# Kernel tuning notes

Measured on AMD Instinct MI355X. Metric: run time of the kernel, lower is better.

## Reference

```python
import jax, jax.numpy as jnp
import numpy as np

B, T, H, I, OUT = 128, 1440, 512, 2, 1
TAU, ALPHA = 6.0, 0.1


def setup_inputs() -> dict:
    key = jax.random.key(0)
    ks = jax.random.split(key, 8)
    xs = jax.random.normal(ks[0], (B, T), dtype=jnp.float32)
    # sparse 0/1 observation mask (channel 2); channel 1 unused by forward
    mask = (jax.random.uniform(ks[1], (B, T)) < 0.05).astype(jnp.float32)
    inp = jnp.stack([xs, jnp.zeros((B, T), jnp.float32), mask], axis=1)[..., None]  # [B,3,T,1]
    s = 1.0 / np.sqrt(H)
    u = lambda k, shp: jax.random.uniform(k, shp, minval=-s, maxval=s, dtype=jnp.float32)
    return {
        "input": inp,
        "w_ih": u(ks[2], (3 * H, I)),
        "w_hh": u(ks[3], (3 * H, H)),
        "b_ih": u(ks[4], (3 * H,)),
        "b_hh": u(ks[5], (3 * H,)),
        "w_fc": u(ks[6], (OUT, H)),
        "b_fc": u(ks[7], (OUT,)),
    }


def belief_fill(x, mask, half_tau):
    # Vectorized equivalent of the per-batch / per-observed-index Python loop:
    # each position takes the value of the next observed index if within half_tau
    # else the previous observed index if within half_tau, else stays unchanged.
    Ts = x.shape[1]
    t = jnp.arange(Ts)[None, :]
    obs = mask == 1
    p = jax.lax.cummax(jnp.where(obs, t, -1), axis=1)                       # prev observed idx or -1
    n = jax.lax.cummin(jnp.where(obs, t, Ts)[:, ::-1], axis=1)[:, ::-1]      # next observed idx or Ts
    xp = jnp.take_along_axis(x, jnp.clip(p, 0, Ts - 1), axis=1)
    xn = jnp.take_along_axis(x, jnp.clip(n, 0, Ts - 1), axis=1)
    use_n = (n < Ts) & (t >= n - half_tau)
    use_p = (p >= 0) & (t <= p + half_tau)
    return jnp.where(use_n, xn, jnp.where(use_p, xp, x))


def _forward(inp, w_ih, w_hh, b_ih, b_hh, w_fc, b_fc):
    xs = inp[:, 0, :, 0]      # [B,T]
    masks = inp[:, 2, :, 0]   # [B,T]
    xs = jnp.where(jnp.isnan(xs), -1.0, xs)
    # tau update: old_weight is ones(3H, I)
    grads = jnp.mean(w_ih - 1.0)
    tau_new = TAU + grads * ALPHA
    trigger = (tau_new >= 1.0) & (tau_new != TAU)
    half_tau = jnp.round(tau_new / 2.0)
    xs = jnp.where(trigger, belief_fill(xs, masks, half_tau), xs)
    gru_in = jnp.stack((xs, masks), axis=2)  # [B,T,2]
    # precompute input projections once (the only input-dependent GEMM)
    gi = jnp.einsum('bti,gi->btg', gru_in, w_ih) + b_ih  # [B,T,3H]

    def step(h, gi_t):
        gh = h @ w_hh.T + b_hh
        r = jax.nn.sigmoid(gi_t[:, :H] + gh[:, :H])
        z = jax.nn.sigmoid(gi_t[:, H:2 * H] + gh[:, H:2 * H])
        ng = jnp.tanh(gi_t[:, 2 * H:] + r * gh[:, 2 * H:])
        h = (1.0 - z) * ng + z * h
        return h, None

    h0 = jnp.zeros((inp.shape[0], H), gi.dtype)
    h_last, _ = jax.lax.scan(step, h0, jnp.swapaxes(gi, 0, 1))
    return h_last @ w_fc.T + b_fc  # [B, OUT]


def reference(input, w_ih, w_hh, b_ih, b_hh, w_fc, b_fc):
    return _forward(input, w_ih, w_hh, b_ih, b_hh, w_fc, b_fc)
```

## Files before the change

### kernel.cpp

```cpp
#include <hip/hip_runtime.h>
#include <math.h>

#define BN   128
#define TN   1440
#define HN   512
#define GBn  8
#define BSn  16
#define GCn  32
#define HCn  16
#define WST  536

using f16 = _Float16;
typedef f16   f16x8 __attribute__((ext_vector_type(8)));
typedef float f32x4 __attribute__((ext_vector_type(4)));
typedef unsigned int       uint32;
typedef unsigned long long u64;

#define OFF_SCAL 1024
#define OFF_HBUF 2048
#define OFF_XSF  (2048 + 2 * BN * HN * 4)

__global__ void k_prep(const float* __restrict__ w_ih, float* __restrict__ scal) {
    __shared__ float ssum[4];
    float s = 0.0f;
    for (int i = threadIdx.x; i < 3 * HN * 2; i += 256) s += w_ih[i];
    for (int o = 32; o >= 1; o >>= 1) s += __shfl_down(s, o, 64);
    if ((threadIdx.x & 63) == 0) ssum[threadIdx.x >> 6] = s;
    __syncthreads();
    if (threadIdx.x == 0) {
        float tot = ssum[0] + ssum[1] + ssum[2] + ssum[3];
        float grads = tot / 3072.0f - 1.0f;
        float tau_new = 6.0f + grads * 0.1f;
        bool trig = (tau_new >= 1.0f) && (tau_new != 6.0f);
        scal[0] = rintf(tau_new * 0.5f);
        scal[1] = trig ? 1.0f : 0.0f;
    }
}

__global__ void k_fill(const float* __restrict__ inp, const float* __restrict__ scal,
                       float* __restrict__ xsf) {
    const int b = blockIdx.x;
    const int lane = threadIdx.x;
    const float ht = scal[0];
    const bool trig = scal[1] != 0.0f;
    const float* xrow = inp + (size_t)b * 3 * TN;
    const float* mrow = xrow + 2 * TN;
    const int CH = 23;
    const int start = lane * CH;

    if (!trig) {
        for (int i = 0; i < CH; ++i) {
            int t = start + i;
            if (t < TN) { float x = xrow[t]; if (x != x) x = -1.0f; xsf[(size_t)b * TN + t] = x; }
        }
        return;
    }
    int pm = -1;
#pragma unroll
    for (int i = 0; i < CH; ++i) { int t = start + i; if (t < TN && mrow[t] == 1.0f) pm = t; }
    int incl = pm;
    for (int o = 1; o < 64; o <<= 1) { int v = __shfl_up(incl, o, 64); if (lane >= o) incl = max(incl, v); }
    int pexcl = __shfl_up(incl, 1, 64); if (lane == 0) pexcl = -1;
    int nm = TN;
#pragma unroll
    for (int i = CH - 1; i >= 0; --i) { int t = start + i; if (t < TN && mrow[t] == 1.0f) nm = t; }
    int incl2 = nm;
    for (int o = 1; o < 64; o <<= 1) { int v = __shfl_down(incl2, o, 64); if (lane + o < 64) incl2 = min(incl2, v); }
    int nexcl = __shfl_down(incl2, 1, 64); if (lane == 63) nexcl = TN;
    int narr[23];
    int runn = nexcl;
#pragma unroll
    for (int i = CH - 1; i >= 0; --i) {
        int t = start + i;
        if (t < TN) { if (mrow[t] == 1.0f) runn = t; narr[i] = runn; } else narr[i] = TN;
    }
    int runp = pexcl;
#pragma unroll
    for (int i = 0; i < CH; ++i) {
        int t = start + i;
        if (t >= TN) break;
        float x = xrow[t]; if (x != x) x = -1.0f;
        if (mrow[t] == 1.0f) runp = t;
        int pv = runp, nv = narr[i];
        int pc = min(max(pv, 0), TN - 1), nc = min(max(nv, 0), TN - 1);
        float xp = xrow[pc]; if (xp != xp) xp = -1.0f;
        float xn = xrow[nc]; if (xn != xn) xn = -1.0f;
        bool use_n = (nv < TN) && ((float)t >= (float)nv - ht);
        bool use_p = (pv >= 0) && ((float)t <= (float)pv + ht);
        float o = use_n ? xn : (use_p ? xp : x);
        xsf[(size_t)b * TN + t] = o;
    }
}

__global__ __launch_bounds__(256, 1) void k_gru(
    const float* __restrict__ inp, const float* __restrict__ w_ih,
    const float* __restrict__ w_hh, const float* __restrict__ b_ih,
    const float* __restrict__ b_hh, const float* __restrict__ w_fc,
    const float* __restrict__ b_fc, const float* __restrict__ xsf,
    uint32* __restrict__ hbufP, int* __restrict__ flags, float* __restrict__ out) {
    __shared__ __align__(16) f16 sHhi[BSn * WST];
    __shared__ __align__(16) f16 sHlo[BSn * WST];
    __shared__ float sGh[3][BSn][HCn + 1];
    __shared__ float sWi0[48], sWi1[48], sBias[48];

    const int tid = threadIdx.x;
    const int gb = blockIdx.x & 7;
    const int gc = blockIdx.x >> 3;
    const int lane = tid & 63;
    const int wv   = tid >> 6;
    const int bs   = tid >> 4;
    const int j    = tid & 15;
    const int bglob = gb * BSn + bs;
    const int pcol  = gc * HCn + j;
    const int frow = lane & 15;
    const int kgrp = lane >> 4;

    if (tid < 48) {
        int gate = tid >> 4, jj = tid & 15;
        int grow = gate * HN + gc * HCn + jj;
        sWi0[tid]  = w_ih[grow * 2 + 0];
        sWi1[tid]  = w_ih[grow * 2 + 1];
        sBias[tid] = b_ih[grow] + b_hh[grow];
    }

    f16x8 bfh[16], bfl[16];
    if (wv < 3) {
        const float* wrow = w_hh + (size_t)(wv * HN + gc * HCn + frow) * HN;
#pragma unroll
        for (int c = 0; c < 16; ++c) {
            const int k0 = (c * 4 + kgrp) * 8;
#pragma unroll
            for (int u = 0; u < 8; ++u) {
                float w = wrow[k0 + u];
                f16 hi = (f16)w;
                bfh[c][u] = hi;
                bfl[c][u] = (f16)((w - (float)hi) * 2048.0f);
            }
        }
    }
    __syncthreads();

    int* myflags = flags + gb * GCn;
    const f16x8* pAhi = (const f16x8*)(sHhi + frow * WST);
    const f16x8* pAlo = (const f16x8*)(sHlo + frow * WST);
    float h = 0.0f;

    for (int t = 0; t < TN; ++t) {
        float xsv = xsf[(size_t)bglob * TN + t];
        float mkv = inp[((size_t)bglob * 3 + 2) * TN + t];
        if (lane < GCn) {
            while (__hip_atomic_load(&myflags[lane], __ATOMIC_RELAXED, __HIP_MEMORY_SCOPE_AGENT) < t) {}
        }
        {
            const uint32* src = hbufP + ((size_t)(t & 1) * BN + gb * BSn) * HN;
            u64 hv[16];
#pragma unroll
            for (int i = 0; i < 16; ++i)
                hv[i] = __hip_atomic_load((const u64*)(src + (size_t)i * HN) + tid,
                                          __ATOMIC_RELAXED, __HIP_MEMORY_SCOPE_AGENT);
#pragma unroll
            for (int i = 0; i < 16; ++i) {
                uint32 d0 = (uint32)hv[i], d1 = (uint32)(hv[i] >> 32);
                ((uint32*)(sHhi + i * WST))[tid] = __builtin_amdgcn_perm(d1, d0, 0x05040100u);
                ((uint32*)(sHlo + i * WST))[tid] = __builtin_amdgcn_perm(d1, d0, 0x07060302u);
            }
        }
        __syncthreads();
        if (wv < 3) {
            f32x4 acch = {0.f, 0.f, 0.f, 0.f}, accl = {0.f, 0.f, 0.f, 0.f};
#pragma unroll
            for (int c = 0; c < 16; ++c) {
                f16x8 ah = pAhi[c * 4 + kgrp];
                f16x8 al = pAlo[c * 4 + kgrp];
                acch = __builtin_amdgcn_mfma_f32_16x16x32_f16(ah, bfh[c], acch, 0, 0, 0);
                accl = __builtin_amdgcn_mfma_f32_16x16x32_f16(ah, bfl[c], accl, 0, 0, 0);
                accl = __builtin_amdgcn_mfma_f32_16x16x32_f16(al, bfh[c], accl, 0, 0, 0);
            }
#pragma unroll
            for (int r = 0; r < 4; ++r)
                sGh[wv][kgrp * 4 + r][frow] = acch[r] + accl[r] * (1.0f / 2048.0f);
        }
        __syncthreads();
        {
            float ghr = sGh[0][bs][j], ghz = sGh[1][bs][j], ghn = sGh[2][bs][j];
            float gir = xsv * sWi0[j]      + mkv * sWi1[j]      + sBias[j];
            float giz = xsv * sWi0[16 + j] + mkv * sWi1[16 + j] + sBias[16 + j];
            float gin = xsv * sWi0[32 + j] + mkv * sWi1[32 + j] + sBias[32 + j];
            float rg = 1.0f / (1.0f + __expf(-(gir + ghr)));
            float zg = 1.0f / (1.0f + __expf(-(giz + ghz)));
            float ng = tanhf(gin + rg * ghn);
            h = (1.0f - zg) * ng + zg * h;
            f16 hi = (f16)h;
            f16 lo = (f16)((h - (float)hi) * 2048.0f);
            uint32 pk = (uint32)__builtin_bit_cast(unsigned short, hi)
                      | ((uint32)__builtin_bit_cast(unsigned short, lo) << 16);
            __hip_atomic_store(&hbufP[((size_t)((t + 1) & 1) * BN + bglob) * HN + pcol], pk,
                               __ATOMIC_RELAXED, __HIP_MEMORY_SCOPE_AGENT);
        }
        __syncthreads();
        if (tid == 0)
            __hip_atomic_store(&myflags[gc], t + 1, __ATOMIC_RELAXED, __HIP_MEMORY_SCOPE_AGENT);
    }
    float part = h * w_fc[pcol];
#pragma unroll
    for (int o = 1; o < 16; o <<= 1) part += __shfl_xor(part, o, 64);
    if (j == 0) {
        if (gc == 0) part += b_fc[0];
        atomicAdd(&out[bglob], part);
    }
}

extern "C" void kernel_launch(void* const* d_in, const int* in_sizes, int n_in,
                              void* d_out, int out_size, void* d_ws, size_t ws_size,
                              hipStream_t stream) {
    const float* inp  = (const float*)d_in[0];
    const float* w_ih = (const float*)d_in[1];
    const float* w_hh = (const float*)d_in[2];
    const float* b_ih = (const float*)d_in[3];
    const float* b_hh = (const float*)d_in[4];
    const float* w_fc = (const float*)d_in[5];
    const float* b_fc = (const float*)d_in[6];
    float* out = (float*)d_out;
    char* ws = (char*)d_ws;
    int*    flags = (int*)ws;
    float*  scal  = (float*)(ws + OFF_SCAL);
    uint32* hbufP = (uint32*)(ws + OFF_HBUF);
    float*  xsf   = (float*)(ws + OFF_XSF);

    hipMemsetAsync(ws, 0, OFF_HBUF + BN * HN * 4, stream);
    hipMemsetAsync(d_out, 0, BN * sizeof(float), stream);
    k_prep<<<1, 256, 0, stream>>>(w_ih, scal);
    k_fill<<<BN, 64, 0, stream>>>(inp, scal, xsf);
    k_gru<<<GBn * GCn, 256, 0, stream>>>(inp, w_ih, w_hh, b_ih, b_hh, w_fc, b_fc,
                                         xsf, hbufP, flags, out);
}
```

Baseline: 3.975 ms.

## Replace per-block step flags with tagged hidden-state words for synchronization

Drops the per-block flag array and the spin-wait/flag-store handshake. Each hidden-state word now packs a 24-bit fixed-point value with an 8-bit step tag, and consumers poll the data itself until the tags match, then convert to hi/lo fp16 pairs. This removes one __syncthreads, one flag round-trip per step and the serialized flag polling. The cost is lower precision for h (24-bit fixed point over [-1,1]), extra conversion arithmetic, and reliance on 64-bit atomic loads so that both tags in a word pair are seen together.

```diff
diff --git a/kernel.cpp b/kernel.cpp
--- a/kernel.cpp
+++ b/kernel.cpp
@@ -97,7 +97,7 @@
     const float* __restrict__ w_hh, const float* __restrict__ b_ih,
     const float* __restrict__ b_hh, const float* __restrict__ w_fc,
     const float* __restrict__ b_fc, const float* __restrict__ xsf,
-    uint32* __restrict__ hbufP, int* __restrict__ flags, float* __restrict__ out) {
+    uint32* __restrict__ hbufT, float* __restrict__ out) {
     __shared__ __align__(16) f16 sHhi[BSn * WST];
     __shared__ __align__(16) f16 sHlo[BSn * WST];
     __shared__ float sGh[3][BSn][HCn + 1];
@@ -140,7 +140,6 @@
     }
     __syncthreads();
 
-    int* myflags = flags + gb * GCn;
     const f16x8* pAhi = (const f16x8*)(sHhi + frow * WST);
     const f16x8* pAlo = (const f16x8*)(sHlo + frow * WST);
     float h = 0.0f;
@@ -148,21 +147,39 @@
     for (int t = 0; t < TN; ++t) {
         float xsv = xsf[(size_t)bglob * TN + t];
         float mkv = inp[((size_t)bglob * 3 + 2) * TN + t];
-        if (lane < GCn) {
-            while (__hip_atomic_load(&myflags[lane], __ATOMIC_RELAXED, __HIP_MEMORY_SCOPE_AGENT) < t) {}
-        }
         {
-            const uint32* src = hbufP + ((size_t)(t & 1) * BN + gb * BSn) * HN;
+            const uint32* src = hbufT + ((size_t)(t & 1) * BN + gb * BSn) * HN;
+            const uint32 tagexp = (uint32)(t & 255);
             u64 hv[16];
 #pragma unroll
-            for (int i = 0; i < 16; ++i)
-                hv[i] = __hip_atomic_load((const u64*)(src + (size_t)i * HN) + tid,
+            for (int i = 0; i < 16; ++i) {
+                int row = (i + bs) & 15;
+                hv[i] = __hip_atomic_load((const u64*)(src + (size_t)row * HN) + tid,
                                           __ATOMIC_RELAXED, __HIP_MEMORY_SCOPE_AGENT);
+            }
 #pragma unroll
             for (int i = 0; i < 16; ++i) {
-                uint32 d0 = (uint32)hv[i], d1 = (uint32)(hv[i] >> 32);
-                ((uint32*)(sHhi + i * WST))[tid] = __builtin_amdgcn_perm(d1, d0, 0x05040100u);
-                ((uint32*)(sHlo + i * WST))[tid] = __builtin_amdgcn_perm(d1, d0, 0x07060302u);
+                int row = (i + bs) & 15;
+                while ((((uint32)hv[i] >> 24) != tagexp) ||
+                       (((uint32)(hv[i] >> 32) >> 24) != tagexp)) {
+                    __builtin_amdgcn_s_sleep(1);
+                    hv[i] = __hip_atomic_load((const u64*)(src + (size_t)row * HN) + tid,
+                                              __ATOMIC_RELAXED, __HIP_MEMORY_SCOPE_AGENT);
+                }
+                uint32 a = (uint32)hv[i], b = (uint32)(hv[i] >> 32);
+                int q0 = ((int)(a << 8)) >> 8;
+                int q1 = ((int)(b << 8)) >> 8;
+                float f0 = (float)q0 * 0x1p-23f;
+                float f1 = (float)q1 * 0x1p-23f;
+                f16 h0 = (f16)f0, h1 = (f16)f1;
+                f16 l0 = (f16)((f0 - (float)h0) * 2048.0f);
+                f16 l1 = (f16)((f1 - (float)h1) * 2048.0f);
+                ((uint32*)(sHhi + row * WST))[tid] =
+                    (uint32)__builtin_bit_cast(unsigned short, h0) |
+                    ((uint32)__builtin_bit_cast(unsigned short, h1) << 16);
+                ((uint32*)(sHlo + row * WST))[tid] =
+                    (uint32)__builtin_bit_cast(unsigned short, l0) |
+                    ((uint32)__builtin_bit_cast(unsigned short, l1) << 16);
             }
         }
         __syncthreads();
@@ -190,16 +207,12 @@
             float zg = 1.0f / (1.0f + __expf(-(giz + ghz)));
             float ng = tanhf(gin + rg * ghn);
             h = (1.0f - zg) * ng + zg * h;
-            f16 hi = (f16)h;
-            f16 lo = (f16)((h - (float)hi) * 2048.0f);
-            uint32 pk = (uint32)__builtin_bit_cast(unsigned short, hi)
-                      | ((uint32)__builtin_bit_cast(unsigned short, lo) << 16);
-            __hip_atomic_store(&hbufP[((size_t)((t + 1) & 1) * BN + bglob) * HN + pcol], pk,
+            int q = (int)rintf(h * 8388608.0f);
+            q = min(q, 8388607);
+            uint32 pk = ((uint32)q & 0xFFFFFFu) | (((uint32)(t + 1) & 255u) << 24);
+            __hip_atomic_store(&hbufT[((size_t)((t + 1) & 1) * BN + bglob) * HN + pcol], pk,
                                __ATOMIC_RELAXED, __HIP_MEMORY_SCOPE_AGENT);
         }
-        __syncthreads();
-        if (tid == 0)
-            __hip_atomic_store(&myflags[gc], t + 1, __ATOMIC_RELAXED, __HIP_MEMORY_SCOPE_AGENT);
     }
     float part = h * w_fc[pcol];
 #pragma unroll
@@ -222,9 +235,8 @@
     const float* b_fc = (const float*)d_in[6];
     float* out = (float*)d_out;
     char* ws = (char*)d_ws;
-    int*    flags = (int*)ws;
     float*  scal  = (float*)(ws + OFF_SCAL);
-    uint32* hbufP = (uint32*)(ws + OFF_HBUF);
+    uint32* hbufT = (uint32*)(ws + OFF_HBUF);
     float*  xsf   = (float*)(ws + OFF_XSF);
 
     hipMemsetAsync(ws, 0, OFF_HBUF + BN * HN * 4, stream);
@@ -232,5 +244,5 @@
     k_prep<<<1, 256, 0, stream>>>(w_ih, scal);
     k_fill<<<BN, 64, 0, stream>>>(inp, scal, xsf);
     k_gru<<<GBn * GCn, 256, 0, stream>>>(inp, w_ih, w_hh, b_ih, b_hh, w_fc, b_fc,
-                                         xsf, hbufP, flags, out);
-}
+                                         xsf, hbufT, out);
+}
```

After: 8.464 ms. 113% more time.

## Collapse GRU block to a single wavefront, loading h directly into registers

Applied to the files above, without the earlier changes.

Each GRU block shrinks from four waves to one 64-thread wave. That wave does all three gate GEMMs with MFMA, keeping the high-half weights in registers and the low-half weights in LDS. The hidden state is now read straight from global memory into registers with inline-asm dwordx4 loads that bypass the cache, and written back with one vector store per thread. This removes the LDS staging of h and all per-step __syncthreads, which shortens the serial per-timestep critical path. The cost is that each wave now does three times the MFMA work, register pressure rises sharply, and ordering depends on hand-written waitcnt asm.

```diff
diff --git a/kernel.cpp b/kernel.cpp
--- a/kernel.cpp
+++ b/kernel.cpp
@@ -8,13 +8,13 @@
 #define BSn  16
 #define GCn  32
 #define HCn  16
-#define WST  536
 
 using f16 = _Float16;
 typedef f16   f16x8 __attribute__((ext_vector_type(8)));
 typedef float f32x4 __attribute__((ext_vector_type(4)));
 typedef unsigned int       uint32;
 typedef unsigned long long u64;
+typedef uint32 u32x4 __attribute__((ext_vector_type(4)));
 
 #define OFF_SCAL 1024
 #define OFF_HBUF 2048
@@ -92,28 +92,23 @@
     }
 }
 
-__global__ __launch_bounds__(256, 1) void k_gru(
+__global__ __launch_bounds__(64, 1) void k_gru(
     const float* __restrict__ inp, const float* __restrict__ w_ih,
     const float* __restrict__ w_hh, const float* __restrict__ b_ih,
     const float* __restrict__ b_hh, const float* __restrict__ w_fc,
     const float* __restrict__ b_fc, const float* __restrict__ xsf,
     uint32* __restrict__ hbufP, int* __restrict__ flags, float* __restrict__ out) {
-    __shared__ __align__(16) f16 sHhi[BSn * WST];
-    __shared__ __align__(16) f16 sHlo[BSn * WST];
-    __shared__ float sGh[3][BSn][HCn + 1];
-    __shared__ float sWi0[48], sWi1[48], sBias[48];
-
-    const int tid = threadIdx.x;
-    const int gb = blockIdx.x & 7;
-    const int gc = blockIdx.x >> 3;
-    const int lane = tid & 63;
-    const int wv   = tid >> 6;
-    const int bs   = tid >> 4;
-    const int j    = tid & 15;
-    const int bglob = gb * BSn + bs;
-    const int pcol  = gc * HCn + j;
-    const int frow = lane & 15;
-    const int kgrp = lane >> 4;
+    __shared__ __align__(16) f16x8 sBlo[48 * 65];
+    __shared__ __align__(16) float sGh[3][16][20];
+    __shared__ __align__(16) float sWi0[48], sWi1[48], sBias[48];
+
+    const int tid  = threadIdx.x;
+    const int gb   = blockIdx.x & 7;
+    const int gc   = blockIdx.x >> 3;
+    const int frow = tid & 15;
+    const int kgrp = tid >> 4;
+    const int r    = tid >> 2;
+    const int jq   = (tid & 3) * 4;
 
     if (tid < 48) {
         int gate = tid >> 4, jj = tid & 15;
@@ -123,90 +118,168 @@
         sBias[tid] = b_ih[grow] + b_hh[grow];
     }
 
-    f16x8 bfh[16], bfl[16];
-    if (wv < 3) {
-        const float* wrow = w_hh + (size_t)(wv * HN + gc * HCn + frow) * HN;
+    f16x8 bh[3][16];
+#pragma unroll
+    for (int g = 0; g < 3; ++g) {
+        const float* wrow = w_hh + (size_t)(g * HN + gc * HCn + frow) * HN;
 #pragma unroll
         for (int c = 0; c < 16; ++c) {
             const int k0 = (c * 4 + kgrp) * 8;
+            f16x8 lo;
 #pragma unroll
             for (int u = 0; u < 8; ++u) {
                 float w = wrow[k0 + u];
                 f16 hi = (f16)w;
-                bfh[c][u] = hi;
-                bfl[c][u] = (f16)((w - (float)hi) * 2048.0f);
+                bh[g][c][u] = hi;
+                lo[u] = (f16)((w - (float)hi) * 2048.0f);
             }
-        }
-    }
-    __syncthreads();
+            sBlo[(g * 16 + frow) * 65 + c * 4 + kgrp] = lo;
+        }
+    }
+    asm volatile("s_waitcnt lgkmcnt(0)" ::: "memory");
 
     int* myflags = flags + gb * GCn;
-    const f16x8* pAhi = (const f16x8*)(sHhi + frow * WST);
-    const f16x8* pAlo = (const f16x8*)(sHlo + frow * WST);
-    float h = 0.0f;
+    const uint32* srcA = hbufP + (size_t)(gb * BSn + frow) * HN + kgrp * 8;
+    const uint32* srcB = srcA + (size_t)BN * HN;
+    uint32* dstA = hbufP + (size_t)(gb * BSn + r) * HN + gc * HCn + jq;
+    uint32* dstB = dstA + (size_t)BN * HN;
+    float hv[4] = {0.f, 0.f, 0.f, 0.f};
+    int fcache = 0;
 
     for (int t = 0; t < TN; ++t) {
-        float xsv = xsf[(size_t)bglob * TN + t];
-        float mkv = inp[((size_t)bglob * 3 + 2) * TN + t];
-        if (lane < GCn) {
-            while (__hip_atomic_load(&myflags[lane], __ATOMIC_RELAXED, __HIP_MEMORY_SCOPE_AGENT) < t) {}
-        }
+        float xsv = xsf[(size_t)(gb * BSn + r) * TN + t];
+        float mkv = inp[((size_t)(gb * BSn + r) * 3 + 2) * TN + t];
+        if (tid < GCn) {
+            while (fcache < t)
+                fcache = __hip_atomic_load(&myflags[tid], __ATOMIC_RELAXED,
+                                           __HIP_MEMORY_SCOPE_AGENT);
+        }
+        const uint32* src = (t & 1) ? srcB : srcA;
+        u32x4 L[32];
+        asm volatile(
+            "global_load_dwordx4 %0, %32, off sc0 sc1\n\t"
+            "global_load_dwordx4 %1, %32, off offset:16 sc0 sc1\n\t"
+            "global_load_dwordx4 %2, %32, off offset:128 sc0 sc1\n\t"
+            "global_load_dwordx4 %3, %32, off offset:144 sc0 sc1\n\t"
+            "global_load_dwordx4 %4, %32, off offset:256 sc0 sc1\n\t"
+            "global_load_dwordx4 %5, %32, off offset:272 sc0 sc1\n\t"
+            "global_load_dwordx4 %6, %32, off offset:384 sc0 sc1\n\t"
+            "global_load_dwordx4 %7, %32, off offset:400 sc0 sc1\n\t"
+            "global_load_dwordx4 %8, %32, off offset:512 sc0 sc1\n\t"
+            "global_load_dwordx4 %9, %32, off offset:528 sc0 sc1\n\t"
+            "global_load_dwordx4 %10, %32, off offset:640 sc0 sc1\n\t"
+            "global_load_dwordx4 %11, %32, off offset:656 sc0 sc1\n\t"
+            "global_load_dwordx4 %12, %32, off offset:768 sc0 sc1\n\t"
+            "global_load_dwordx4 %13, %32, off offset:784 sc0 sc1\n\t"
+            "global_load_dwordx4 %14, %32, off offset:896 sc0 sc1\n\t"
+            "global_load_dwordx4 %15, %32, off offset:912 sc0 sc1\n\t"
+            "global_load_dwordx4 %16, %32, off offset:1024 sc0 sc1\n\t"
+            "global_load_dwordx4 %17, %32, off offset:1040 sc0 sc1\n\t"
+            "global_load_dwordx4 %18, %32, off offset:1152 sc0 sc1\n\t"
+            "global_load_dwordx4 %19, %32, off offset:1168 sc0 sc1\n\t"
+            "global_load_dwordx4 %20, %32, off offset:1280 sc0 sc1\n\t"
+            "global_load_dwordx4 %21, %32, off offset:1296 sc0 sc1\n\t"
+            "global_load_dwordx4 %22, %32, off offset:1408 sc0 sc1\n\t"
+            "global_load_dwordx4 %23, %32, off offset:1424 sc0 sc1\n\t"
+            "global_load_dwordx4 %24, %32, off offset:1536 sc0 sc1\n\t"
+            "global_load_dwordx4 %25, %32, off offset:1552 sc0 sc1\n\t"
+            "global_load_dwordx4 %26, %32, off offset:1664 sc0 sc1\n\t"
+            "global_load_dwordx4 %27, %32, off offset:1680 sc0 sc1\n\t"
+            "global_load_dwordx4 %28, %32, off offset:1792 sc0 sc1\n\t"
+            "global_load_dwordx4 %29, %32, off offset:1808 sc0 sc1\n\t"
+            "global_load_dwordx4 %30, %32, off offset:1920 sc0 sc1\n\t"
+            "global_load_dwordx4 %31, %32, off offset:1936 sc0 sc1\n\t"
+            "s_waitcnt vmcnt(0)"
+            : "=&v"(L[0]), "=&v"(L[1]), "=&v"(L[2]), "=&v"(L[3]),
+              "=&v"(L[4]), "=&v"(L[5]), "=&v"(L[6]), "=&v"(L[7]),
+              "=&v"(L[8]), "=&v"(L[9]), "=&v"(L[10]), "=&v"(L[11]),
+              "=&v"(L[12]), "=&v"(L[13]), "=&v"(L[14]), "=&v"(L[15]),
+              "=&v"(L[16]), "=&v"(L[17]), "=&v"(L[18]), "=&v"(L[19]),
+              "=&v"(L[20]), "=&v"(L[21]), "=&v"(L[22]), "=&v"(L[23]),
+              "=&v"(L[24]), "=&v"(L[25]), "=&v"(L[26]), "=&v"(L[27]),
+              "=&v"(L[28]), "=&v"(L[29]), "=&v"(L[30]), "=&v"(L[31])
+            : "v"(src)
+            : "memory");
+        f32x4 acch[3]  = {{0.f,0.f,0.f,0.f},{0.f,0.f,0.f,0.f},{0.f,0.f,0.f,0.f}};
+        f32x4 accl1[3] = {{0.f,0.f,0.f,0.f},{0.f,0.f,0.f,0.f},{0.f,0.f,0.f,0.f}};
+        f32x4 accl2[3] = {{0.f,0.f,0.f,0.f},{0.f,0.f,0.f,0.f},{0.f,0.f,0.f,0.f}};
+#pragma unroll
+        for (int c = 0; c < 16; ++c) {
+            u32x4 a = L[2 * c], b = L[2 * c + 1];
+            u32x4 hq = { __builtin_amdgcn_perm(a.y, a.x, 0x05040100u),
+                         __builtin_amdgcn_perm(a.w, a.z, 0x05040100u),
+                         __builtin_amdgcn_perm(b.y, b.x, 0x05040100u),
+                         __builtin_amdgcn_perm(b.w, b.z, 0x05040100u) };
+            u32x4 lq = { __builtin_amdgcn_perm(a.y, a.x, 0x07060302u),
+                         __builtin_amdgcn_perm(a.w, a.z, 0x07060302u),
+                         __builtin_amdgcn_perm(b.y, b.x, 0x07060302u),
+                         __builtin_amdgcn_perm(b.w, b.z, 0x07060302u) };
+            f16x8 ah = __builtin_bit_cast(f16x8, hq);
+            f16x8 al = __builtin_bit_cast(f16x8, lq);
+#pragma unroll
+            for (int g = 0; g < 3; ++g) {
+                f16x8 bl = sBlo[(g * 16 + frow) * 65 + c * 4 + kgrp];
+                acch[g]  = __builtin_amdgcn_mfma_f32_16x16x32_f16(ah, bh[g][c], acch[g], 0, 0, 0);
+                accl1[g] = __builtin_amdgcn_mfma_f32_16x16x32_f16(ah, bl,       accl1[g], 0, 0, 0);
+                accl2[g] = __builtin_amdgcn_mfma_f32_16x16x32_f16(al, bh[g][c], accl2[g], 0, 0, 0);
+            }
+        }
+#pragma unroll
+        for (int g = 0; g < 3; ++g)
+#pragma unroll
+            for (int q = 0; q < 4; ++q)
+                sGh[g][kgrp * 4 + q][frow] =
+                    acch[g][q] + (accl1[g][q] + accl2[g][q]) * (1.0f / 2048.0f);
+        asm volatile("s_waitcnt lgkmcnt(0)" ::: "memory");
+        float4 gr = *(const float4*)&sGh[0][r][jq];
+        float4 gz = *(const float4*)&sGh[1][r][jq];
+        float4 gn = *(const float4*)&sGh[2][r][jq];
+        float4 w0r = *(const float4*)&sWi0[jq],      w1r = *(const float4*)&sWi1[jq],      bbr = *(const float4*)&sBias[jq];
+        float4 w0z = *(const float4*)&sWi0[16 + jq], w1z = *(const float4*)&sWi1[16 + jq], bbz = *(const float4*)&sBias[16 + jq];
+        float4 w0n = *(const float4*)&sWi0[32 + jq], w1n = *(const float4*)&sWi1[32 + jq], bbn = *(const float4*)&sBias[32 + jq];
+        uint32 pk[4];
         {
-            const uint32* src = hbufP + ((size_t)(t & 1) * BN + gb * BSn) * HN;
-            u64 hv[16];
-#pragma unroll
-            for (int i = 0; i < 16; ++i)
-                hv[i] = __hip_atomic_load((const u64*)(src + (size_t)i * HN) + tid,
-                                          __ATOMIC_RELAXED, __HIP_MEMORY_SCOPE_AGENT);
-#pragma unroll
-            for (int i = 0; i < 16; ++i) {
-                uint32 d0 = (uint32)hv[i], d1 = (uint32)(hv[i] >> 32);
-                ((uint32*)(sHhi + i * WST))[tid] = __builtin_amdgcn_perm(d1, d0, 0x05040100u);
-                ((uint32*)(sHlo + i * WST))[tid] = __builtin_amdgcn_perm(d1, d0, 0x07060302u);
+            const float* grp = (const float*)&gr; const float* gzp = (const float*)&gz;
+            const float* gnp = (const float*)&gn;
+            const float* a0r = (const float*)&w0r; const float* a1r = (const float*)&w1r; const float* abr = (const float*)&bbr;
+            const float* a0z = (const float*)&w0z; const float* a1z = (const float*)&w1z; const float* abz = (const float*)&bbz;
+            const float* a0n = (const float*)&w0n; const float* a1n = (const float*)&w1n; const float* abn = (const float*)&bbn;
+#pragma unroll
+            for (int i = 0; i < 4; ++i) {
+                float gir = fmaf(xsv, a0r[i], fmaf(mkv, a1r[i], abr[i])) + grp[i];
+                float giz = fmaf(xsv, a0z[i], fmaf(mkv, a1z[i], abz[i])) + gzp[i];
+                float gin = fmaf(xsv, a0n[i], fmaf(mkv, a1n[i], abn[i]));
+                float rg = 1.0f / (1.0f + __expf(-gir));
+                float zg = 1.0f / (1.0f + __expf(-giz));
+                float ng = tanhf(gin + rg * gnp[i]);
+                float hn2 = (1.0f - zg) * ng + zg * hv[i];
+                hv[i] = hn2;
+                f16 phi = (f16)hn2;
+                f16 plo = (f16)((hn2 - (float)phi) * 2048.0f);
+                pk[i] = (uint32)__builtin_bit_cast(unsigned short, phi)
+                      | ((uint32)__builtin_bit_cast(unsigned short, plo) << 16);
             }
         }
-        __syncthreads();
-        if (wv < 3) {
-            f32x4 acch = {0.f, 0.f, 0.f, 0.f}, accl = {0.f, 0.f, 0.f, 0.f};
-#pragma unroll
-            for (int c = 0; c < 16; ++c) {
-                f16x8 ah = pAhi[c * 4 + kgrp];
-                f16x8 al = pAlo[c * 4 + kgrp];
-                acch = __builtin_amdgcn_mfma_f32_16x16x32_f16(ah, bfh[c], acch, 0, 0, 0);
-                accl = __builtin_amdgcn_mfma_f32_16x16x32_f16(ah, bfl[c], accl, 0, 0, 0);
-                accl = __builtin_amdgcn_mfma_f32_16x16x32_f16(al, bfh[c], accl, 0, 0, 0);
-            }
-#pragma unroll
-            for (int r = 0; r < 4; ++r)
-                sGh[wv][kgrp * 4 + r][frow] = acch[r] + accl[r] * (1.0f / 2048.0f);
-        }
-        __syncthreads();
         {
-            float ghr = sGh[0][bs][j], ghz = sGh[1][bs][j], ghn = sGh[2][bs][j];
-            float gir = xsv * sWi0[j]      + mkv * sWi1[j]      + sBias[j];
-            float giz = xsv * sWi0[16 + j] + mkv * sWi1[16 + j] + sBias[16 + j];
-            float gin = xsv * sWi0[32 + j] + mkv * sWi1[32 + j] + sBias[32 + j];
-            float rg = 1.0f / (1.0f + __expf(-(gir + ghr)));
-            float zg = 1.0f / (1.0f + __expf(-(giz + ghz)));
-            float ng = tanhf(gin + rg * ghn);
-            h = (1.0f - zg) * ng + zg * h;
-            f16 hi = (f16)h;
-            f16 lo = (f16)((h - (float)hi) * 2048.0f);
-            uint32 pk = (uint32)__builtin_bit_cast(unsigned short, hi)
-                      | ((uint32)__builtin_bit_cast(unsigned short, lo) << 16);
-            __hip_atomic_store(&hbufP[((size_t)((t + 1) & 1) * BN + bglob) * HN + pcol], pk,
-                               __ATOMIC_RELAXED, __HIP_MEMORY_SCOPE_AGENT);
-        }
-        __syncthreads();
+            u32x4 val = { pk[0], pk[1], pk[2], pk[3] };
+            uint32* dst = (t & 1) ? dstA : dstB;
+            asm volatile(
+                "global_store_dwordx4 %0, %1, off sc0 sc1\n\t"
+                "s_waitcnt vmcnt(0)"
+                :: "v"(dst), "v"(val)
+                : "memory");
+        }
         if (tid == 0)
-            __hip_atomic_store(&myflags[gc], t + 1, __ATOMIC_RELAXED, __HIP_MEMORY_SCOPE_AGENT);
-    }
-    float part = h * w_fc[pcol];
-#pragma unroll
-    for (int o = 1; o < 16; o <<= 1) part += __shfl_xor(part, o, 64);
-    if (j == 0) {
+            __hip_atomic_store(&myflags[gc], t + 1, __ATOMIC_RELAXED,
+                               __HIP_MEMORY_SCOPE_AGENT);
+    }
+    const float* wf = w_fc + gc * HCn + jq;
+    float part = hv[0] * wf[0] + hv[1] * wf[1] + hv[2] * wf[2] + hv[3] * wf[3];
+    part += __shfl_xor(part, 1, 64);
+    part += __shfl_xor(part, 2, 64);
+    if ((tid & 3) == 0) {
         if (gc == 0) part += b_fc[0];
-        atomicAdd(&out[bglob], part);
+        atomicAdd(&out[gb * BSn + r], part);
     }
 }
 
@@ -231,6 +304,6 @@
     hipMemsetAsync(d_out, 0, BN * sizeof(float), stream);
     k_prep<<<1, 256, 0, stream>>>(w_ih, scal);
     k_fill<<<BN, 64, 0, stream>>>(inp, scal, xsf);
-    k_gru<<<GBn * GCn, 256, 0, stream>>>(inp, w_ih, w_hh, b_ih, b_hh, w_fc, b_fc,
-                                         xsf, hbufP, flags, out);
+    k_gru<<<GBn * GCn, 64, 0, stream>>>(inp, w_ih, w_hh, b_ih, b_hh, w_fc, b_fc,
+                                        xsf, hbufP, flags, out);
 }
```

Measured after the change: 7.057 ms. 77.5% more time.
